# Optimization experiments

Measured on AMD Instinct MI355X. Metric: run time of the kernel, lower is better.

Reference implementation:

```python
import jax, jax.numpy as jnp
import numpy as np

HID = 50
IN_DIM = 20
OUT_DIM = 8


def lstm_cell(x, h, c, Wih, Whh, bih, bhh):
    # PyTorch LSTMCell: gates ordered i, f, g, o
    gates = x @ Wih.T + bih + h @ Whh.T + bhh  # [B, 4*HID]
    i, f, g, o = jnp.split(gates, 4, axis=-1)
    i = jax.nn.sigmoid(i)
    f = jax.nn.sigmoid(f)
    g = jnp.tanh(g)
    o = jax.nn.sigmoid(o)
    c_new = f * c + i * g
    h_new = o * jnp.tanh(c_new)
    return h_new, c_new


def setup_inputs() -> dict:
    key = jax.random.key(0)
    ks = jax.random.split(key, 16)
    s = 1.0 / np.sqrt(HID)
    u = lambda k, shape, bound: jax.random.uniform(k, shape, jnp.float32, -bound, bound)
    inp = {
        "x": jax.random.normal(ks[0], (512, 1024, IN_DIM), jnp.float32),
        "W1": u(ks[1], (HID, IN_DIM), 1.0 / np.sqrt(IN_DIM)),
        "b1": u(ks[2], (HID,), 1.0 / np.sqrt(IN_DIM)),
        "Wih1": u(ks[3], (4 * HID, HID), s), "Whh1": u(ks[4], (4 * HID, HID), s),
        "bih1": u(ks[5], (4 * HID,), s), "bhh1": u(ks[6], (4 * HID,), s),
        "Wih2": u(ks[7], (4 * HID, HID), s), "Whh2": u(ks[8], (4 * HID, HID), s),
        "bih2": u(ks[9], (4 * HID,), s), "bhh2": u(ks[10], (4 * HID,), s),
        "Wih3": u(ks[11], (4 * HID, HID), s), "Whh3": u(ks[12], (4 * HID, HID), s),
        "bih3": u(ks[13], (4 * HID,), s), "bhh3": u(ks[14], (4 * HID,), s),
        "W2": u(ks[15], (OUT_DIM, HID), s),
        "b2": jnp.zeros((OUT_DIM,), jnp.float32),
    }
    return inp


def reference(x, W1, b1, Wih1, Whh1, bih1, bhh1, Wih2, Whh2, bih2, bhh2,
              Wih3, Whh3, bih3, bhh3, W2, b2):
    B, T, _ = x.shape
    # Precompute the input projection for all timesteps (linear1)
    hid_all = x @ W1.T + b1  # [B, T, HID]
    z = jnp.zeros((B, HID), x.dtype)
    # carry replicates the original's (buggy) state handling:
    #   h3, c2 = lstm3(h2, (h3, c3)); c3 is never updated (stays zero)
    def step(carry, hid_t):
        h1, c1, h2, c2, h3, c3 = carry
        h1, c1 = lstm_cell(hid_t, h1, c1, Wih1, Whh1, bih1, bhh1)
        h2, c2 = lstm_cell(h1, h2, c2, Wih2, Whh2, bih2, bhh2)
        h3, c2 = lstm_cell(h2, h3, c3, Wih3, Whh3, bih3, bhh3)
        out = h3 @ W2.T + b2
        return (h1, c1, h2, c2, h3, c3), out

    _, outs = jax.lax.scan(step, (z, z, z, z, z, z),
                           jnp.swapaxes(hid_all, 0, 1))  # scan over time
    return jnp.swapaxes(outs, 0, 1)  # [B, T, OUT_DIM]
```

## Files before the change

### kernel.cpp

```cpp
#include <hip/hip_runtime.h>


#define T_SEQ 1024
#define HID   50
#define IN_DIM 20
#define OUT_DIM 8

typedef float f32x2 __attribute__((ext_vector_type(2)));
typedef float f32x4 __attribute__((ext_vector_type(4)));

__device__ __forceinline__ void pkfma_lo(f32x2& d, f32x2 w, f32x2 u) {
    asm("v_pk_fma_f32 %0, %1, %2, %0 op_sel:[0,0,0] op_sel_hi:[0,1,1]"
        : "+v"(d) : "v"(w), "v"(u));
}
__device__ __forceinline__ void pkfma_hi(f32x2& d, f32x2 w, f32x2 u) {
    asm("v_pk_fma_f32 %0, %1, %2, %0 op_sel:[1,0,0] op_sel_hi:[1,1,1]"
        : "+v"(d) : "v"(w), "v"(u));
}
__device__ __forceinline__ float sigm(float x) {
    return __builtin_amdgcn_rcpf(1.0f + __expf(-x));
}
__device__ __forceinline__ float tanh_f(float x) {
    return fmaf(2.0f, sigm(2.0f * x), -1.0f);
}
template <int CTRL>
__device__ __forceinline__ f32x2 dpp2(f32x2 v) {
    f32x2 r;
    r.x = __int_as_float(__builtin_amdgcn_mov_dpp(__float_as_int(v.x), CTRL, 0xF, 0xF, true));
    r.y = __int_as_float(__builtin_amdgcn_mov_dpp(__float_as_int(v.y), CTRL, 0xF, 0xF, true));
    return r;
}
__device__ __forceinline__ f32x2 swzx4(f32x2 v) {
    f32x2 r;
    r.x = __int_as_float(__builtin_amdgcn_ds_swizzle(__float_as_int(v.x), 0x101F));
    r.y = __int_as_float(__builtin_amdgcn_ds_swizzle(__float_as_int(v.y), 0x101F));
    return r;
}

__global__ __launch_bounds__(704, 2) void lstm_net_kernel(
    const float* __restrict__ x,
    const float* __restrict__ W1,   const float* __restrict__ b1,
    const float* __restrict__ Wih1, const float* __restrict__ Whh1,
    const float* __restrict__ bih1, const float* __restrict__ bhh1,
    const float* __restrict__ Wih2, const float* __restrict__ Whh2,
    const float* __restrict__ bih2, const float* __restrict__ bhh2,
    const float* __restrict__ Wih3, const float* __restrict__ Whh3,
    const float* __restrict__ bih3, const float* __restrict__ bhh3,
    const float* __restrict__ W2,   const float* __restrict__ b2,
    float* __restrict__ out)
{
    __shared__ __align__(16) f32x2 sm2[390];
    f32x2* xr  = sm2;
    f32x2* h1b = sm2 + 78;
    f32x2* h2b = sm2 + 182;
    f32x2* h3b = sm2 + 286;

    const int tid = threadIdx.x;
    const int b0  = blockIdx.x * 2;

    for (int i = tid; i < 390; i += 704) sm2[i] = (f32x2){0.f, 0.f};
    __syncthreads();

    f32x2 wv[52];
    float bias4[4] = {0.f, 0.f, 0.f, 0.f};
    int   bsel = 0, boff = 0;
    bool  isGate = false, isL1 = false, isL2 = false, isL3 = false, wr = false;
    int   unit = 0, ok = 0, sk = 0;
    f32x2 c1 = {0.f, 0.f}, xstg = {0.f, 0.f};

    #pragma unroll
    for (int i = 0; i < 52; i++) wv[i] = (f32x2){0.f, 0.f};

    if (tid < 640) {
        isGate = true;
        int r, layer;
        if (tid < 400) {
            unit = tid >> 3; const int r8 = tid & 7;
            isL2 = (r8 < 4); isL3 = !isL2; r = r8 & 3;
            layer = isL2 ? 2 : 3;
            wr = (r8 == 0) || (r8 == 4);
        } else {
            unit = (tid - 400) >> 2; r = tid & 3; isL1 = true; layer = 1;
            wr = ((tid & 3) == 0) && (unit < 50);
        }
        if (layer == 2)      { bsel = (r < 2) ? 1 : 2; boff = 26 * (r & 1); }
        else if (layer == 3) { bsel = (r < 2) ? 2 : 3; boff = 26 * (r & 1); }
        else                 { bsel = (r == 0) ? 0 : 1; boff = (r == 0) ? 0 : 18 * (r - 1); }

        if (unit < 50) {
            const int row[4] = {unit, 50 + unit, 100 + unit, 150 + unit};
            if (layer >= 2) {
                const float* src = (layer == 2) ? ((r < 2) ? Wih2 : Whh2)
                                                : ((r < 2) ? Wih3 : Whh3);
                const float* bi = (layer == 2) ? bih2 : bih3;
                const float* bh = (layer == 2) ? bhh2 : bhh3;
                #pragma unroll
                for (int m = 0; m < 4; m++) {
                    if (layer == 3 && m == 1) continue;
                    bias4[m] = bi[row[m]] + bh[row[m]];
                    #pragma unroll
                    for (int i = 0; i < 13; i++) {
                        const int e0 = 26 * (r & 1) + 2 * i, e1 = e0 + 1;
                        float w0 = (e0 < 50) ? src[row[m] * 50 + e0] : 0.f;
                        float w1 = (e1 < 50) ? src[row[m] * 50 + e1] : 0.f;
                        wv[m * 13 + i] = (f32x2){w0, w1};
                    }
                }
            } else {
                #pragma unroll
                for (int m = 0; m < 4; m++) {
                    float bs = bih1[row[m]] + bhh1[row[m]];
                    for (int j2 = 0; j2 < 50; j2++)
                        bs = fmaf(Wih1[row[m] * 50 + j2], b1[j2], bs);
                    bias4[m] = bs;
                }
                if (r == 0) {
                    #pragma unroll
                    for (int m = 0; m < 4; m++) {
                        float a20[20];
                        #pragma unroll
                        for (int k = 0; k < 20; k++) a20[k] = 0.f;
                        for (int j2 = 0; j2 < 50; j2++) {
                            const float a = Wih1[row[m] * 50 + j2];
                            const float* w1r = W1 + j2 * 20;
                            #pragma unroll
                            for (int k = 0; k < 20; k++)
                                a20[k] = fmaf(a, w1r[k], a20[k]);
                        }
                        #pragma unroll
                        for (int i = 0; i < 10; i++)
                            wv[m * 13 + i] = (f32x2){a20[2 * i], a20[2 * i + 1]};
                    }
                } else {
                    const int off = 18 * (r - 1);
                    const int ecap = (r == 3) ? 14 : 18;
                    #pragma unroll
                    for (int m = 0; m < 4; m++)
                    #pragma unroll
                    for (int i = 0; i < 13; i++) {
                        const int e0 = 2 * i, e1 = e0 + 1;
                        float w0 = (e0 < ecap) ? Whh1[row[m] * 50 + off + e0] : 0.f;
                        float w1 = (e1 < ecap) ? Whh1[row[m] * 50 + off + e1] : 0.f;
                        wv[m * 13 + i] = (f32x2){w0, w1};
                    }
                }
            }
        }
    } else if (tid < 648) {
        ok = tid - 640;
        #pragma unroll
        for (int i = 0; i < 26; i++) {
            const int e0 = 2 * i, e1 = e0 + 1;
            float w0 = (e0 < 50) ? W2[ok * 50 + e0] : 0.f;
            float w1 = (e1 < 50) ? W2[ok * 50 + e1] : 0.f;
            wv[i] = (f32x2){w0, w1};
        }
        bias4[0] = b2[ok];
    } else if (tid < 668) {
        sk = tid - 648;
        #pragma unroll
        for (int t = 0; t < 3; t++) {
            f32x2 v;
            v.x = x[((size_t)b0 * T_SEQ + t) * IN_DIM + sk];
            v.y = x[((size_t)(b0 + 1) * T_SEQ + t) * IN_DIM + sk];
            if (t < 2) xr[t * 26 + sk] = v; else xstg = v;
        }
    }
    __syncthreads();

    for (int s = 0; s < T_SEQ + 3; ++s) {
        const int p = s & 1, pm = p ^ 1, q3 = s % 3;

        if (isGate) {
            const f32x2* base =
                (bsel == 0) ? (xr + q3 * 26) :
                (bsel == 1) ? (h1b + pm * 52) :
                (bsel == 2) ? (h2b + p * 52) : (h3b + pm * 52);
            base += boff;
            const f32x4* B4 = (const f32x4*)base;
            f32x2 a0 = {0.f,0.f}, a1 = {0.f,0.f}, a2 = {0.f,0.f}, a3 = {0.f,0.f};
            #pragma unroll
            for (int i = 0; i < 13; i++) {
                const f32x4 u = B4[i];
                const f32x2 ul = {u.x, u.y}, uh = {u.z, u.w};
                pkfma_lo(a0, wv[i],      ul); pkfma_hi(a0, wv[i],      uh);
                pkfma_lo(a1, wv[13 + i], ul); pkfma_hi(a1, wv[13 + i], uh);
                pkfma_lo(a2, wv[26 + i], ul); pkfma_hi(a2, wv[26 + i], uh);
                pkfma_lo(a3, wv[39 + i], ul); pkfma_hi(a3, wv[39 + i], uh);
            }
            a0 += dpp2<0xB1>(a0); a0 += dpp2<0x4E>(a0);
            a1 += dpp2<0xB1>(a1); a1 += dpp2<0x4E>(a1);
            a2 += dpp2<0xB1>(a2); a2 += dpp2<0x4E>(a2);
            a3 += dpp2<0xB1>(a3); a3 += dpp2<0x4E>(a3);

            f32x2 ii = {sigm(a0.x + bias4[0]),   sigm(a0.y + bias4[0])};
            f32x2 ff = {sigm(a1.x + bias4[1]),   sigm(a1.y + bias4[1])};
            f32x2 gg = {tanh_f(a2.x + bias4[2]), tanh_f(a2.y + bias4[2])};
            f32x2 oo = {sigm(a3.x + bias4[3]),   sigm(a3.y + bias4[3])};
            f32x2 ig = ii * gg;

            const bool valid3 = (s >= 2) && (s < T_SEQ + 2);
            f32x2 ps = ig;
            if (isL3 && !valid3) ps = (f32x2){0.f, 0.f};
            const f32x2 pr = swzx4(ps);

            if (isL1) {
                if (s < T_SEQ) {
                    c1.x = fmaf(ff.x, c1.x, ig.x);
                    c1.y = fmaf(ff.y, c1.y, ig.y);
                    if (wr) {
                        f32x2 h;
                        h.x = oo.x * tanh_f(c1.x); h.y = oo.y * tanh_f(c1.y);
                        h1b[p * 52 + unit] = h;
                    }
                }
            } else if (isL2) {
                if (s >= 1 && s <= T_SEQ) {
                    f32x2 c2;
                    c2.x = fmaf(ff.x, pr.x, ig.x);
                    c2.y = fmaf(ff.y, pr.y, ig.y);
                    if (wr) {
                        f32x2 h;
                        h.x = oo.x * tanh_f(c2.x); h.y = oo.y * tanh_f(c2.y);
                        h2b[pm * 52 + unit] = h;
                    }
                }
            } else {
                if (valid3 && wr) {
                    f32x2 h;
                    h.x = oo.x * tanh_f(ig.x); h.y = oo.y * tanh_f(ig.y);
                    h3b[p * 52 + unit] = h;
                }
            }
        } else if (tid < 648) {
            if (s >= 3) {
                const f32x4* H4 = (const f32x4*)(h3b + pm * 52);
                f32x2 acc = {0.f, 0.f};
                #pragma unroll
                for (int i = 0; i < 26; i++) {
                    const f32x4 u = H4[i];
                    const f32x2 ul = {u.x, u.y}, uh = {u.z, u.w};
                    pkfma_lo(acc, wv[i], ul);
                    pkfma_hi(acc, wv[i], uh);
                }
                const int t = s - 3;
                out[((size_t)b0 * T_SEQ + t) * OUT_DIM + ok]       = acc.x + bias4[0];
                out[((size_t)(b0 + 1) * T_SEQ + t) * OUT_DIM + ok] = acc.y + bias4[0];
            }
        } else if (tid < 668) {
            if (s + 2 < T_SEQ) xr[((s + 2) % 3) * 26 + sk] = xstg;
            if (s + 3 < T_SEQ) {
                xstg.x = x[((size_t)b0 * T_SEQ + (s + 3)) * IN_DIM + sk];
                xstg.y = x[((size_t)(b0 + 1) * T_SEQ + (s + 3)) * IN_DIM + sk];
            }
        }
        __syncthreads();
    }
}

extern "C" void kernel_launch(void* const* d_in, const int* in_sizes, int n_in,
                              void* d_out, int out_size, void* d_ws, size_t ws_size,
                              hipStream_t stream) {
    const float* x    = (const float*)d_in[0];
    const float* W1   = (const float*)d_in[1];
    const float* b1   = (const float*)d_in[2];
    const float* Wih1 = (const float*)d_in[3];
    const float* Whh1 = (const float*)d_in[4];
    const float* bih1 = (const float*)d_in[5];
    const float* bhh1 = (const float*)d_in[6];
    const float* Wih2 = (const float*)d_in[7];
    const float* Whh2 = (const float*)d_in[8];
    const float* bih2 = (const float*)d_in[9];
    const float* bhh2 = (const float*)d_in[10];
    const float* Wih3 = (const float*)d_in[11];
    const float* Whh3 = (const float*)d_in[12];
    const float* bih3 = (const float*)d_in[13];
    const float* bhh3 = (const float*)d_in[14];
    const float* W2   = (const float*)d_in[15];
    const float* b2   = (const float*)d_in[16];
    float* out = (float*)d_out;

    dim3 grid(256), block(704);
    lstm_net_kernel<<<grid, block, 0, stream>>>(
        x, W1, b1, Wih1, Whh1, bih1, bhh1, Wih2, Whh2, bih2, bhh2,
        Wih3, Whh3, bih3, bhh3, W2, b2, out);
}
```

Measured before the change: 1.686 ms.

## Repartition LSTM work across 512 threads with wider per-thread dot products

Reduces the block from 704 to 512 threads (8 wavefronts instead of 11) by giving each gate thread 36-element dot-product slices (72 weight pairs) instead of 26. Layer 1 now uses 2 threads per unit over a concatenated [x, h1] buffer, and the x loader uses 4 threads loading 5 dims each. The shared-memory layout is repacked accordingly. The intent is to shrink the per-step barrier cost and wave count on this latency-bound recurrence, at the cost of longer per-thread FMA chains and higher register pressure.

```diff
diff --git a/kernel.cpp b/kernel.cpp
--- a/kernel.cpp
+++ b/kernel.cpp
@@ -2,9 +2,13 @@
 
 
 #define T_SEQ 1024
-#define HID   50
 #define IN_DIM 20
 #define OUT_DIM 8
+
+#define XC   0
+#define XH2  176
+#define XH3  304
+#define SMSZ 432
 
 typedef float f32x2 __attribute__((ext_vector_type(2)));
 typedef float f32x4 __attribute__((ext_vector_type(4)));
@@ -17,11 +21,20 @@
     asm("v_pk_fma_f32 %0, %1, %2, %0 op_sel:[1,0,0] op_sel_hi:[1,1,1]"
         : "+v"(d) : "v"(w), "v"(u));
 }
+__device__ __forceinline__ void pkfma(f32x2& d, f32x2 a, f32x2 b) {
+    asm("v_pk_fma_f32 %0, %1, %2, %0" : "+v"(d) : "v"(a), "v"(b));
+}
 __device__ __forceinline__ float sigm(float x) {
     return __builtin_amdgcn_rcpf(1.0f + __expf(-x));
 }
 __device__ __forceinline__ float tanh_f(float x) {
     return fmaf(2.0f, sigm(2.0f * x), -1.0f);
+}
+__device__ __forceinline__ f32x2 sigm2(f32x2 v, float b) {
+    f32x2 r; r.x = sigm(v.x + b); r.y = sigm(v.y + b); return r;
+}
+__device__ __forceinline__ f32x2 tanh2(f32x2 v, float b) {
+    f32x2 r; r.x = tanh_f(v.x + b); r.y = tanh_f(v.y + b); return r;
 }
 template <int CTRL>
 __device__ __forceinline__ f32x2 dpp2(f32x2 v) {
@@ -37,7 +50,7 @@
     return r;
 }
 
-__global__ __launch_bounds__(704, 2) void lstm_net_kernel(
+__global__ __launch_bounds__(512, 2) void lstm_net_kernel(
     const float* __restrict__ x,
     const float* __restrict__ W1,   const float* __restrict__ b1,
     const float* __restrict__ Wih1, const float* __restrict__ Whh1,
@@ -49,209 +62,205 @@
     const float* __restrict__ W2,   const float* __restrict__ b2,
     float* __restrict__ out)
 {
-    __shared__ __align__(16) f32x2 sm2[390];
-    f32x2* xr  = sm2;
-    f32x2* h1b = sm2 + 78;
-    f32x2* h2b = sm2 + 182;
-    f32x2* h3b = sm2 + 286;
+    __shared__ __align__(16) f32x2 sm2[SMSZ];
 
     const int tid = threadIdx.x;
     const int b0  = blockIdx.x * 2;
 
-    for (int i = tid; i < 390; i += 704) sm2[i] = (f32x2){0.f, 0.f};
+    for (int i = tid; i < SMSZ; i += 512) sm2[i] = (f32x2){0.f, 0.f};
     __syncthreads();
 
-    f32x2 wv[52];
+    f32x2 wv[72];
+    #pragma unroll
+    for (int i = 0; i < 72; i++) wv[i] = (f32x2){0.f, 0.f};
     float bias4[4] = {0.f, 0.f, 0.f, 0.f};
-    int   bsel = 0, boff = 0;
-    bool  isGate = false, isL1 = false, isL2 = false, isL3 = false, wr = false;
-    int   unit = 0, ok = 0, sk = 0;
-    f32x2 c1 = {0.f, 0.f}, xstg = {0.f, 0.f};
-
+    int   sel = 0, boff = 0, u = 0, loc = 0, ok = 0, sd = 0;
+    bool  isOct = false, isL3 = false;
+    f32x2 c1 = {0.f, 0.f};
+    f32x2 xs[5];
     #pragma unroll
-    for (int i = 0; i < 52; i++) wv[i] = (f32x2){0.f, 0.f};
-
-    if (tid < 640) {
-        isGate = true;
-        int r, layer;
-        if (tid < 400) {
-            unit = tid >> 3; const int r8 = tid & 7;
-            isL2 = (r8 < 4); isL3 = !isL2; r = r8 & 3;
-            layer = isL2 ? 2 : 3;
-            wr = (r8 == 0) || (r8 == 4);
-        } else {
-            unit = (tid - 400) >> 2; r = tid & 3; isL1 = true; layer = 1;
-            wr = ((tid & 3) == 0) && (unit < 50);
-        }
-        if (layer == 2)      { bsel = (r < 2) ? 1 : 2; boff = 26 * (r & 1); }
-        else if (layer == 3) { bsel = (r < 2) ? 2 : 3; boff = 26 * (r & 1); }
-        else                 { bsel = (r == 0) ? 0 : 1; boff = (r == 0) ? 0 : 18 * (r - 1); }
-
-        if (unit < 50) {
-            const int row[4] = {unit, 50 + unit, 100 + unit, 150 + unit};
-            if (layer >= 2) {
-                const float* src = (layer == 2) ? ((r < 2) ? Wih2 : Whh2)
-                                                : ((r < 2) ? Wih3 : Whh3);
-                const float* bi = (layer == 2) ? bih2 : bih3;
-                const float* bh = (layer == 2) ? bhh2 : bhh3;
-                #pragma unroll
-                for (int m = 0; m < 4; m++) {
-                    if (layer == 3 && m == 1) continue;
-                    bias4[m] = bi[row[m]] + bh[row[m]];
+    for (int i = 0; i < 5; i++) xs[i] = (f32x2){0.f, 0.f};
+
+    if (tid < 400) {
+        isOct = true;
+        u = tid >> 3; loc = tid & 7; isL3 = (loc >= 4);
+        const int r = loc & 3, side = r >> 1, chunk = r & 1;
+        const float* src = isL3 ? (side ? Whh3 : Wih3) : (side ? Whh2 : Wih2);
+        const float* bi  = isL3 ? bih3 : bih2;
+        const float* bh  = isL3 ? bhh3 : bhh2;
+        const int row4[4] = {u, 50 + u, 100 + u, 150 + u};
+        #pragma unroll
+        for (int m = 0; m < 4; m++) {
+            const bool dead = isL3 && (m == 1);
+            const int row = row4[m];
+            #pragma unroll
+            for (int i = 0; i < 18; i++) {
+                const int k0 = 2 * i, k1 = 2 * i + 1;
+                const int d0 = 26 * chunk + k0, d1 = 26 * chunk + k1;
+                const float w0 = (!dead && k0 < 26 && d0 < 50) ? src[row * 50 + d0] : 0.f;
+                const float w1 = (!dead && k1 < 26 && d1 < 50) ? src[row * 50 + d1] : 0.f;
+                wv[m * 18 + i] = (f32x2){w0, w1};
+            }
+            bias4[m] = dead ? 0.f : bi[row] + bh[row];
+        }
+        if (!isL3) { sel = side ? 1 : 0; boff = side ? 26 * chunk : 20 + 26 * chunk; }
+        else       { sel = side ? 2 : 1; boff = 26 * chunk; }
+    } else if (tid < 500) {
+        u = (tid - 400) >> 1;
+        const int h = tid & 1;
+        sel = 0; boff = 36 * h;
+        const int row4[4] = {u, 50 + u, 100 + u, 150 + u};
+        #pragma unroll
+        for (int m = 0; m < 4; m++) {
+            const int row = row4[m];
+            float bs = bih1[row] + bhh1[row];
+            for (int j = 0; j < 50; j++) bs = fmaf(Wih1[row * 50 + j], b1[j], bs);
+            bias4[m] = bs;
+            if (h == 0) {
+                float a20[20];
+                #pragma unroll
+                for (int k = 0; k < 20; k++) a20[k] = 0.f;
+                for (int j = 0; j < 50; j++) {
+                    const float a = Wih1[row * 50 + j];
+                    const float* w1r = W1 + j * 20;
                     #pragma unroll
-                    for (int i = 0; i < 13; i++) {
-                        const int e0 = 26 * (r & 1) + 2 * i, e1 = e0 + 1;
-                        float w0 = (e0 < 50) ? src[row[m] * 50 + e0] : 0.f;
-                        float w1 = (e1 < 50) ? src[row[m] * 50 + e1] : 0.f;
-                        wv[m * 13 + i] = (f32x2){w0, w1};
-                    }
+                    for (int k = 0; k < 20; k++) a20[k] = fmaf(a, w1r[k], a20[k]);
+                }
+                #pragma unroll
+                for (int i = 0; i < 18; i++) {
+                    const int k0 = 2 * i, k1 = 2 * i + 1;
+                    const float w0 = (k0 < 20) ? a20[k0] : Whh1[row * 50 + (k0 - 20)];
+                    const float w1 = (k1 < 20) ? a20[k1] : Whh1[row * 50 + (k1 - 20)];
+                    wv[m * 18 + i] = (f32x2){w0, w1};
                 }
             } else {
                 #pragma unroll
-                for (int m = 0; m < 4; m++) {
-                    float bs = bih1[row[m]] + bhh1[row[m]];
-                    for (int j2 = 0; j2 < 50; j2++)
-                        bs = fmaf(Wih1[row[m] * 50 + j2], b1[j2], bs);
-                    bias4[m] = bs;
-                }
-                if (r == 0) {
-                    #pragma unroll
-                    for (int m = 0; m < 4; m++) {
-                        float a20[20];
-                        #pragma unroll
-                        for (int k = 0; k < 20; k++) a20[k] = 0.f;
-                        for (int j2 = 0; j2 < 50; j2++) {
-                            const float a = Wih1[row[m] * 50 + j2];
-                            const float* w1r = W1 + j2 * 20;
-                            #pragma unroll
-                            for (int k = 0; k < 20; k++)
-                                a20[k] = fmaf(a, w1r[k], a20[k]);
-                        }
-                        #pragma unroll
-                        for (int i = 0; i < 10; i++)
-                            wv[m * 13 + i] = (f32x2){a20[2 * i], a20[2 * i + 1]};
-                    }
-                } else {
-                    const int off = 18 * (r - 1);
-                    const int ecap = (r == 3) ? 14 : 18;
-                    #pragma unroll
-                    for (int m = 0; m < 4; m++)
-                    #pragma unroll
-                    for (int i = 0; i < 13; i++) {
-                        const int e0 = 2 * i, e1 = e0 + 1;
-                        float w0 = (e0 < ecap) ? Whh1[row[m] * 50 + off + e0] : 0.f;
-                        float w1 = (e1 < ecap) ? Whh1[row[m] * 50 + off + e1] : 0.f;
-                        wv[m * 13 + i] = (f32x2){w0, w1};
-                    }
-                }
-            }
-        }
-    } else if (tid < 648) {
-        ok = tid - 640;
+                for (int i = 0; i < 18; i++) {
+                    const int k0 = 2 * i, k1 = 2 * i + 1;
+                    const float w0 = (k0 < 34) ? Whh1[row * 50 + 16 + k0] : 0.f;
+                    const float w1 = (k1 < 34) ? Whh1[row * 50 + 16 + k1] : 0.f;
+                    wv[m * 18 + i] = (f32x2){w0, w1};
+                }
+            }
+        }
+    } else if (tid < 508) {
+        ok = tid - 500;
         #pragma unroll
         for (int i = 0; i < 26; i++) {
-            const int e0 = 2 * i, e1 = e0 + 1;
-            float w0 = (e0 < 50) ? W2[ok * 50 + e0] : 0.f;
-            float w1 = (e1 < 50) ? W2[ok * 50 + e1] : 0.f;
+            const int d0 = 2 * i, d1 = 2 * i + 1;
+            const float w0 = (d0 < 50) ? W2[ok * 50 + d0] : 0.f;
+            const float w1 = (d1 < 50) ? W2[ok * 50 + d1] : 0.f;
             wv[i] = (f32x2){w0, w1};
         }
         bias4[0] = b2[ok];
-    } else if (tid < 668) {
-        sk = tid - 648;
-        #pragma unroll
+    } else {
+        sd = tid - 508;
         for (int t = 0; t < 3; t++) {
-            f32x2 v;
-            v.x = x[((size_t)b0 * T_SEQ + t) * IN_DIM + sk];
-            v.y = x[((size_t)(b0 + 1) * T_SEQ + t) * IN_DIM + sk];
-            if (t < 2) xr[t * 26 + sk] = v; else xstg = v;
+            #pragma unroll
+            for (int i = 0; i < 5; i++) {
+                const int dim = sd + 4 * i;
+                f32x2 v;
+                v.x = x[((size_t)b0 * T_SEQ + t) * IN_DIM + dim];
+                v.y = x[((size_t)(b0 + 1) * T_SEQ + t) * IN_DIM + dim];
+                if (t < 2) sm2[XC + t * 88 + dim] = v;
+                else       xs[i] = v;
+            }
         }
     }
     __syncthreads();
 
     for (int s = 0; s < T_SEQ + 3; ++s) {
-        const int p = s & 1, pm = p ^ 1, q3 = s % 3;
-
-        if (isGate) {
-            const f32x2* base =
-                (bsel == 0) ? (xr + q3 * 26) :
-                (bsel == 1) ? (h1b + pm * 52) :
-                (bsel == 2) ? (h2b + p * 52) : (h3b + pm * 52);
-            base += boff;
-            const f32x4* B4 = (const f32x4*)base;
-            f32x2 a0 = {0.f,0.f}, a1 = {0.f,0.f}, a2 = {0.f,0.f}, a3 = {0.f,0.f};
+        const int p = s & 1, pm = p ^ 1;
+
+        if (tid < 500) {
+            const int base = ((sel == 0) ? (XC + p * 88)
+                            : (sel == 1) ? (XH2 + p * 64)
+                                         : (XH3 + pm * 64)) + boff;
+            const f32x4* B4 = (const f32x4*)(sm2 + base);
+            f32x2 A0 = {0.f,0.f}, A1 = {0.f,0.f}, A2 = {0.f,0.f}, A3 = {0.f,0.f};
             #pragma unroll
-            for (int i = 0; i < 13; i++) {
-                const f32x4 u = B4[i];
-                const f32x2 ul = {u.x, u.y}, uh = {u.z, u.w};
-                pkfma_lo(a0, wv[i],      ul); pkfma_hi(a0, wv[i],      uh);
-                pkfma_lo(a1, wv[13 + i], ul); pkfma_hi(a1, wv[13 + i], uh);
-                pkfma_lo(a2, wv[26 + i], ul); pkfma_hi(a2, wv[26 + i], uh);
-                pkfma_lo(a3, wv[39 + i], ul); pkfma_hi(a3, wv[39 + i], uh);
-            }
-            a0 += dpp2<0xB1>(a0); a0 += dpp2<0x4E>(a0);
-            a1 += dpp2<0xB1>(a1); a1 += dpp2<0x4E>(a1);
-            a2 += dpp2<0xB1>(a2); a2 += dpp2<0x4E>(a2);
-            a3 += dpp2<0xB1>(a3); a3 += dpp2<0x4E>(a3);
-
-            f32x2 ii = {sigm(a0.x + bias4[0]),   sigm(a0.y + bias4[0])};
-            f32x2 ff = {sigm(a1.x + bias4[1]),   sigm(a1.y + bias4[1])};
-            f32x2 gg = {tanh_f(a2.x + bias4[2]), tanh_f(a2.y + bias4[2])};
-            f32x2 oo = {sigm(a3.x + bias4[3]),   sigm(a3.y + bias4[3])};
-            f32x2 ig = ii * gg;
-
-            const bool valid3 = (s >= 2) && (s < T_SEQ + 2);
-            f32x2 ps = ig;
-            if (isL3 && !valid3) ps = (f32x2){0.f, 0.f};
-            const f32x2 pr = swzx4(ps);
-
-            if (isL1) {
-                if (s < T_SEQ) {
-                    c1.x = fmaf(ff.x, c1.x, ig.x);
-                    c1.y = fmaf(ff.y, c1.y, ig.y);
-                    if (wr) {
-                        f32x2 h;
-                        h.x = oo.x * tanh_f(c1.x); h.y = oo.y * tanh_f(c1.y);
-                        h1b[p * 52 + unit] = h;
+            for (int i = 0; i < 18; i++) {
+                const f32x4 uu = B4[i];
+                const f32x2 ul = uu.lo, uh = uu.hi;
+                pkfma_lo(A0, wv[i],      ul); pkfma_hi(A0, wv[i],      uh);
+                pkfma_lo(A1, wv[18 + i], ul); pkfma_hi(A1, wv[18 + i], uh);
+                pkfma_lo(A2, wv[36 + i], ul); pkfma_hi(A2, wv[36 + i], uh);
+                pkfma_lo(A3, wv[54 + i], ul); pkfma_hi(A3, wv[54 + i], uh);
+            }
+            A0 += dpp2<0xB1>(A0); A1 += dpp2<0xB1>(A1);
+            A2 += dpp2<0xB1>(A2); A3 += dpp2<0xB1>(A3);
+            if (isOct) {
+                A0 += dpp2<0x4E>(A0); A1 += dpp2<0x4E>(A1);
+                A2 += dpp2<0x4E>(A2); A3 += dpp2<0x4E>(A3);
+            }
+            const f32x2 ii = sigm2(A0, bias4[0]);
+            const f32x2 ff = sigm2(A1, bias4[1]);
+            const f32x2 gg = tanh2(A2, bias4[2]);
+            const f32x2 oo = sigm2(A3, bias4[3]);
+            f32x2 P = ii * gg;
+
+            if (isOct) {
+                const bool valid3 = (s >= 2) && (s < T_SEQ + 2);
+                f32x2 ps = P;
+                if (isL3 && !valid3) ps = (f32x2){0.f, 0.f};
+                const f32x2 t4 = swzx4(ps);
+                if (loc == 0) {
+                    if (s >= 1 && s <= T_SEQ) {
+                        f32x2 c2 = P;
+                        pkfma(c2, ff, t4);
+                        f32x2 hh;
+                        hh.x = oo.x * tanh_f(c2.x);
+                        hh.y = oo.y * tanh_f(c2.y);
+                        sm2[XH2 + pm * 64 + u] = hh;
                     }
-                }
-            } else if (isL2) {
-                if (s >= 1 && s <= T_SEQ) {
-                    f32x2 c2;
-                    c2.x = fmaf(ff.x, pr.x, ig.x);
-                    c2.y = fmaf(ff.y, pr.y, ig.y);
-                    if (wr) {
-                        f32x2 h;
-                        h.x = oo.x * tanh_f(c2.x); h.y = oo.y * tanh_f(c2.y);
-                        h2b[pm * 52 + unit] = h;
+                } else if (loc == 4) {
+                    if (valid3) {
+                        f32x2 hh;
+                        hh.x = oo.x * tanh_f(P.x);
+                        hh.y = oo.y * tanh_f(P.y);
+                        sm2[XH3 + p * 64 + u] = hh;
                     }
                 }
             } else {
-                if (valid3 && wr) {
-                    f32x2 h;
-                    h.x = oo.x * tanh_f(ig.x); h.y = oo.y * tanh_f(ig.y);
-                    h3b[p * 52 + unit] = h;
-                }
-            }
-        } else if (tid < 648) {
+                if ((tid & 1) == 0 && s < T_SEQ) {
+                    f32x2 cn = P;
+                    pkfma(cn, ff, c1);
+                    c1 = cn;
+                    f32x2 hh;
+                    hh.x = oo.x * tanh_f(c1.x);
+                    hh.y = oo.y * tanh_f(c1.y);
+                    sm2[XC + pm * 88 + 20 + u] = hh;
+                }
+            }
+        } else if (tid < 508) {
             if (s >= 3) {
-                const f32x4* H4 = (const f32x4*)(h3b + pm * 52);
-                f32x2 acc = {0.f, 0.f};
+                const int t = s - 3;
+                const f32x4* H4 = (const f32x4*)(sm2 + XH3 + pm * 64);
+                f32x2 a0 = {0.f, 0.f}, a1 = {0.f, 0.f};
                 #pragma unroll
                 for (int i = 0; i < 26; i++) {
-                    const f32x4 u = H4[i];
-                    const f32x2 ul = {u.x, u.y}, uh = {u.z, u.w};
-                    pkfma_lo(acc, wv[i], ul);
-                    pkfma_hi(acc, wv[i], uh);
-                }
-                const int t = s - 3;
+                    const f32x4 uu = H4[i];
+                    pkfma_lo(a0, wv[i], uu.lo);
+                    pkfma_hi(a1, wv[i], uu.hi);
+                }
+                const f32x2 acc = a0 + a1;
                 out[((size_t)b0 * T_SEQ + t) * OUT_DIM + ok]       = acc.x + bias4[0];
                 out[((size_t)(b0 + 1) * T_SEQ + t) * OUT_DIM + ok] = acc.y + bias4[0];
             }
-        } else if (tid < 668) {
-            if (s + 2 < T_SEQ) xr[((s + 2) % 3) * 26 + sk] = xstg;
-            if (s + 3 < T_SEQ) {
-                xstg.x = x[((size_t)b0 * T_SEQ + (s + 3)) * IN_DIM + sk];
-                xstg.y = x[((size_t)(b0 + 1) * T_SEQ + (s + 3)) * IN_DIM + sk];
+        } else {
+            if (s >= 1 && s + 1 < T_SEQ) {
+                #pragma unroll
+                for (int i = 0; i < 5; i++)
+                    sm2[XC + pm * 88 + sd + 4 * i] = xs[i];
+            }
+            if (s + 2 < T_SEQ) {
+                const int t = s + 2;
+                #pragma unroll
+                for (int i = 0; i < 5; i++) {
+                    const int dim = sd + 4 * i;
+                    xs[i].x = x[((size_t)b0 * T_SEQ + t) * IN_DIM + dim];
+                    xs[i].y = x[((size_t)(b0 + 1) * T_SEQ + t) * IN_DIM + dim];
+                }
             }
         }
         __syncthreads();
@@ -280,7 +289,7 @@
     const float* b2   = (const float*)d_in[16];
     float* out = (float*)d_out;
 
-    dim3 grid(256), block(704);
+    dim3 grid(256), block(512);
     lstm_net_kernel<<<grid, block, 0, stream>>>(
         x, W1, b1, Wih1, Whh1, bih1, bhh1, Wih2, Whh2, bih2, bhh2,
         Wih3, Whh3, bih3, bhh3, W2, b2, out);
```

Measured after the change: 1.730 ms. 1.03x slower.
